# Optimization experiments

Measured on AMD Instinct MI355X. Metric: run time of the kernel, lower is better.

The kernel has to match this reference:

```python
import jax, jax.numpy as jnp
import numpy as np

IN_FEAT = 512
D_FEAT = 512
N_HEAD = 8
EPS = 1e-5
NEG = -1e9


def setup_inputs() -> dict:
    key = jax.random.key(0)
    ks = jax.random.split(key, 12)
    B, C, T = 8, IN_FEAT, 2048
    s_in = 1.0 / np.sqrt(IN_FEAT)
    s_d = 1.0 / np.sqrt(D_FEAT)
    return {
        "x": jax.random.normal(ks[0], (B, C, T), dtype=jnp.float32),
        "gamma": jnp.ones((IN_FEAT,), dtype=jnp.float32),
        "beta": jnp.zeros((IN_FEAT,), dtype=jnp.float32),
        "wq": jax.random.uniform(ks[1], (IN_FEAT, D_FEAT), jnp.float32, -s_in, s_in),
        "bq": jax.random.uniform(ks[2], (D_FEAT,), jnp.float32, -s_in, s_in),
        "wk": jax.random.uniform(ks[3], (IN_FEAT, D_FEAT), jnp.float32, -s_in, s_in),
        "bk": jax.random.uniform(ks[4], (D_FEAT,), jnp.float32, -s_in, s_in),
        "wv": jax.random.uniform(ks[5], (IN_FEAT, D_FEAT), jnp.float32, -s_in, s_in),
        "bv": jax.random.uniform(ks[6], (D_FEAT,), jnp.float32, -s_in, s_in),
        "wo": jax.random.uniform(ks[7], (D_FEAT, IN_FEAT), jnp.float32, -s_d, s_d),
        "bo": jax.random.uniform(ks[8], (IN_FEAT,), jnp.float32, -s_d, s_d),
    }


def reference(x, gamma, beta, wq, bq, wk, bk, wv, bv, wo, bo):
    # x: (B, Cin, T)
    resi = x
    h = jnp.swapaxes(x, -2, -1)  # (B, T, Cin)
    mu = jnp.mean(h, axis=-1, keepdims=True)
    var = jnp.mean(jnp.square(h - mu), axis=-1, keepdims=True)
    h = (h - mu) / jnp.sqrt(var + EPS) * gamma + beta

    B, T, _ = h.shape
    dh = D_FEAT // N_HEAD
    scale = np.sqrt(dh).astype(np.float32)

    def split_heads(y):  # (B,T,D) -> (B,H,T,dh)
        return jnp.swapaxes(y.reshape(B, T, N_HEAD, dh), 1, 2)

    q = split_heads(h @ wq + bq)
    k = split_heads(h @ wk + bk)
    v = split_heads(h @ wv + bv)

    scores = jnp.einsum('bhqd,bhkd->bhqk', q, k) / scale  # (B,H,T,T)
    mask = jnp.triu(jnp.ones((T, T), dtype=scores.dtype), k=1)  # strict upper
    scores = scores + NEG * mask
    attn = jax.nn.softmax(scores, axis=-1)
    ctx = jnp.einsum('bhqk,bhkd->bhqd', attn, v)  # (B,H,T,dh)
    ctx = jnp.swapaxes(ctx, 1, 2).reshape(B, T, D_FEAT)
    out = jnp.swapaxes(ctx @ wo + bo, -2, -1)  # (B, Cin, T)
    return resi + out
```

## Files before the change

kernel.cpp:

```cpp
#include <hip/hip_runtime.h>
#include <hip/hip_bf16.h>

#define BB 8
#define TT 2048
#define CC 512
#define DD 512
#define HH 8
#define DH 64

typedef __bf16 bf16x8 __attribute__((ext_vector_type(8)));
typedef __bf16 bf16x4 __attribute__((ext_vector_type(4)));
typedef float  f32x4  __attribute__((ext_vector_type(4)));

static __device__ __forceinline__ bf16x8 concat4(bf16x4 a, bf16x4 b) {
    bf16x8 r;
    #pragma unroll
    for (int i = 0; i < 4; ++i) { r[i] = a[i]; r[i + 4] = b[i]; }
    return r;
}

__global__ __launch_bounds__(256) void ln_kernel(
    const float* __restrict__ x, const float* __restrict__ gamma,
    const float* __restrict__ beta, __hip_bfloat16* __restrict__ h)
{
    const int b  = blockIdx.x >> 6;
    const int t0 = (blockIdx.x & 63) * 32;
    const int tid = threadIdx.x;
    const int tl = tid & 31;
    const int part = tid >> 5;

    const float* xb = x + (size_t)b * CC * TT;

    float sum = 0.f, sq = 0.f;
    for (int ci = 0; ci < 64; ++ci) {
        int c = part * 64 + ci;
        float v = xb[(size_t)c * TT + t0 + tl];
        sum += v; sq += v * v;
    }
    __shared__ float sA[8][32], sB[8][32];
    sA[part][tl] = sum; sB[part][tl] = sq;
    __syncthreads();
    __shared__ float s_mu[32], s_rstd[32];
    if (part == 0) {
        float s = 0.f, q = 0.f;
        for (int p = 0; p < 8; ++p) { s += sA[p][tl]; q += sB[p][tl]; }
        float mu  = s * (1.0f / 512.0f);
        float var = q * (1.0f / 512.0f) - mu * mu;
        s_mu[tl] = mu;
        s_rstd[tl] = rsqrtf(var + 1e-5f);
    }
    __syncthreads();

    const float mu = s_mu[tl], rstd = s_rstd[tl];
    __shared__ __hip_bfloat16 tileT[32][72];

    for (int chunk = 0; chunk < 8; ++chunk) {
        int cb = chunk * 64 + part * 8;
        #pragma unroll
        for (int j = 0; j < 8; ++j) {
            int c = cb + j;
            float v = xb[(size_t)c * TT + t0 + tl];
            float nv = (v - mu) * rstd * gamma[c] + beta[c];
            tileT[tl][part * 8 + j] = __float2bfloat16(nv);
        }
        __syncthreads();
        int cl = tid & 63, tw = tid >> 6;
        #pragma unroll
        for (int k = 0; k < 8; ++k) {
            int t = tw + k * 4;
            h[((size_t)(b * TT + t0 + t)) * CC + chunk * 64 + cl] = tileT[t][cl];
        }
        __syncthreads();
    }
}

__global__ __launch_bounds__(256) void prepack_w4(
    const float* __restrict__ w0, const float* __restrict__ w1,
    const float* __restrict__ w2, const float* __restrict__ w3,
    __hip_bfloat16* __restrict__ o0, __hip_bfloat16* __restrict__ o1,
    __hip_bfloat16* __restrict__ o2, __hip_bfloat16* __restrict__ o3)
{
    const float* w; __hip_bfloat16* wt;
    switch (blockIdx.y) {
        case 0: w = w0; wt = o0; break;
        case 1: w = w1; wt = o1; break;
        case 2: w = w2; wt = o2; break;
        default: w = w3; wt = o3; break;
    }
    __shared__ float tile[32][33];
    const int bx = blockIdx.x & 15;
    const int by = blockIdx.x >> 4;
    const int lx = threadIdx.x & 31, ly = threadIdx.x >> 5;
    #pragma unroll
    for (int i = 0; i < 4; ++i) {
        int k = by * 32 + ly + i * 8;
        tile[ly + i * 8][lx] = w[(size_t)k * 512 + bx * 32 + lx];
    }
    __syncthreads();
    #pragma unroll
    for (int i = 0; i < 4; ++i) {
        int n = bx * 32 + ly + i * 8;
        wt[(size_t)n * 512 + by * 32 + lx] = __float2bfloat16(tile[lx][ly + i * 8]);
    }
}

__global__ __launch_bounds__(256) void qkv_gemm(
    const __hip_bfloat16* __restrict__ A,
    const __hip_bfloat16* __restrict__ wtq, const __hip_bfloat16* __restrict__ wtk,
    const __hip_bfloat16* __restrict__ wtv,
    const float* __restrict__ bq, const float* __restrict__ bk,
    const float* __restrict__ bv,
    __hip_bfloat16* __restrict__ qo, __hip_bfloat16* __restrict__ ko,
    __hip_bfloat16* __restrict__ vt)
{
    const int m0 = blockIdx.x * 128;
    const int n0 = blockIdx.y * 128;
    const __hip_bfloat16* WT; const float* bias; __hip_bfloat16* out;
    if (blockIdx.z == 0)      { WT = wtq; bias = bq; out = qo; }
    else if (blockIdx.z == 1) { WT = wtk; bias = bk; out = ko; }
    else                      { WT = wtv; bias = bv; out = vt; }
    const float sc = (blockIdx.z == 0) ? 0.18033688011112042f : 1.0f;

    __shared__ __hip_bfloat16 As[2][128][40];
    __shared__ __hip_bfloat16 Bs[2][128][40];
    __shared__ float eps[4][16][17];

    const int tid = threadIdx.x;
    const int wave = tid >> 6, lane = tid & 63;
    const int quad = lane >> 4, l16 = lane & 15;
    const int wy = wave >> 1, wx = wave & 1;

    const int srow = tid >> 2;
    const int skof = (tid & 3) * 8;

    f32x4 acc[4][4] = {};
    bf16x8 areg[2], breg[2];

    #pragma unroll
    for (int i = 0; i < 2; ++i) {
        int r = srow + i * 64;
        areg[i] = *reinterpret_cast<const bf16x8*>(&A[(size_t)(m0 + r) * 512 + skof]);
        breg[i] = *reinterpret_cast<const bf16x8*>(&WT[(size_t)(n0 + r) * 512 + skof]);
    }
    #pragma unroll
    for (int i = 0; i < 2; ++i) {
        int r = srow + i * 64;
        *reinterpret_cast<bf16x8*>(&As[0][r][skof]) = areg[i];
        *reinterpret_cast<bf16x8*>(&Bs[0][r][skof]) = breg[i];
    }
    __syncthreads();

    for (int kt = 0; kt < 512; kt += 32) {
        const int cur = (kt >> 5) & 1;
        const bool havenext = (kt + 32 < 512);
        if (havenext) {
            #pragma unroll
            for (int i = 0; i < 2; ++i) {
                int r = srow + i * 64;
                areg[i] = *reinterpret_cast<const bf16x8*>(
                    &A[(size_t)(m0 + r) * 512 + kt + 32 + skof]);
                breg[i] = *reinterpret_cast<const bf16x8*>(
                    &WT[(size_t)(n0 + r) * 512 + kt + 32 + skof]);
            }
        }
        bf16x8 af[4], bfr[4];
        #pragma unroll
        for (int mt = 0; mt < 4; ++mt)
            af[mt] = *reinterpret_cast<const bf16x8*>(&As[cur][wy * 64 + mt * 16 + l16][quad * 8]);
        #pragma unroll
        for (int nt = 0; nt < 4; ++nt)
            bfr[nt] = *reinterpret_cast<const bf16x8*>(&Bs[cur][wx * 64 + nt * 16 + l16][quad * 8]);
        #pragma unroll
        for (int mt = 0; mt < 4; ++mt)
            #pragma unroll
            for (int nt = 0; nt < 4; ++nt)
                acc[mt][nt] = __builtin_amdgcn_mfma_f32_16x16x32_bf16(
                    af[mt], bfr[nt], acc[mt][nt], 0, 0, 0);
        if (havenext) {
            #pragma unroll
            for (int i = 0; i < 2; ++i) {
                int r = srow + i * 64;
                *reinterpret_cast<bf16x8*>(&As[cur ^ 1][r][skof]) = areg[i];
                *reinterpret_cast<bf16x8*>(&Bs[cur ^ 1][r][skof]) = breg[i];
            }
        }
        __syncthreads();
    }

    if (blockIdx.z != 2) {
        #pragma unroll
        for (int nt = 0; nt < 4; ++nt) {
            int n = n0 + wx * 64 + nt * 16 + l16;
            int hh = n >> 6, di = n & 63;
            float bval = bias[n];
            #pragma unroll
            for (int mt = 0; mt < 4; ++mt) {
                #pragma unroll
                for (int r = 0; r < 4; ++r) {
                    int m = m0 + wy * 64 + mt * 16 + quad * 4 + r;
                    int b = m >> 11, t = m & 2047;
                    out[((size_t)((b * HH + hh) * TT + t)) * DH + di] =
                        __float2bfloat16((acc[mt][nt][r] + bval) * sc);
                }
            }
        }
    } else {
        #pragma unroll
        for (int mt = 0; mt < 4; ++mt) {
            int mbase = m0 + wy * 64 + mt * 16;
            #pragma unroll
            for (int nt = 0; nt < 4; ++nt) {
                int ncol = n0 + wx * 64 + nt * 16 + l16;
                float bval = bias[ncol];
                #pragma unroll
                for (int r = 0; r < 4; ++r)
                    eps[wave][quad * 4 + r][l16] = acc[mt][nt][r] + bval;
                #pragma unroll
                for (int pass = 0; pass < 4; ++pass) {
                    int nl = pass * 4 + quad;
                    int n = n0 + wx * 64 + nt * 16 + nl;
                    int hh = n >> 6, di = n & 63;
                    int m = mbase + l16;
                    int b = m >> 11, t = m & 2047;
                    out[((size_t)((b * HH + hh) * DH + di)) * TT + t] =
                        __float2bfloat16(eps[wave][l16][nl]);
                }
            }
        }
    }
}

static __device__ __forceinline__ void attn_tile(
    const __hip_bfloat16 (*Ksb)[72], const __hip_bfloat16 (*Vtsb)[72],
    int k0, int q0, int wave, int quad, int l16,
    const bf16x8 (&qf)[2][2], f32x4 (&o_acc)[4][2], float (&l_run)[2])
{
    f32x4 s[2][4];
    #pragma unroll
    for (int nt = 0; nt < 4; ++nt) {
        bf16x8 kf0 = *reinterpret_cast<const bf16x8*>(&Ksb[nt * 16 + l16][quad * 8]);
        bf16x8 kf1 = *reinterpret_cast<const bf16x8*>(&Ksb[nt * 16 + l16][32 + quad * 8]);
        #pragma unroll
        for (int mt = 0; mt < 2; ++mt) {
            f32x4 z = {};
            z = __builtin_amdgcn_mfma_f32_16x16x32_bf16(kf0, qf[mt][0], z, 0, 0, 0);
            z = __builtin_amdgcn_mfma_f32_16x16x32_bf16(kf1, qf[mt][1], z, 0, 0, 0);
            s[mt][nt] = z;
        }
    }
    bf16x4 pt[2][4];
    #pragma unroll
    for (int mt = 0; mt < 2; ++mt) {
        const int qrow = q0 + wave * 32 + mt * 16 + l16;
        const bool fullun = (k0 + 63 <= q0 + wave * 32 + mt * 16);
        float lsum = 0.f;
        #pragma unroll
        for (int nt = 0; nt < 4; ++nt) {
            #pragma unroll
            for (int r = 0; r < 4; ++r) {
                float p = __builtin_amdgcn_exp2f(s[mt][nt][r]);
                if (!fullun) {
                    int key = k0 + nt * 16 + quad * 4 + r;
                    if (key > qrow) p = 0.f;
                }
                lsum += p;
                pt[mt][nt][r] = (__bf16)p;
            }
        }
        l_run[mt] += lsum;
    }
    #pragma unroll
    for (int cp = 0; cp < 2; ++cp) {
        bf16x8 pfr[2];
        #pragma unroll
        for (int mt = 0; mt < 2; ++mt)
            pfr[mt] = concat4(pt[mt][cp * 2], pt[mt][cp * 2 + 1]);
        #pragma unroll
        for (int dt = 0; dt < 4; ++dt) {
            bf16x4 va = *reinterpret_cast<const bf16x4*>(
                &Vtsb[dt * 16 + l16][cp * 32 + quad * 4]);
            bf16x4 vb = *reinterpret_cast<const bf16x4*>(
                &Vtsb[dt * 16 + l16][cp * 32 + 16 + quad * 4]);
            bf16x8 vf = concat4(va, vb);
            #pragma unroll
            for (int mt = 0; mt < 2; ++mt)
                o_acc[dt][mt] = __builtin_amdgcn_mfma_f32_16x16x32_bf16(
                    vf, pfr[mt], o_acc[dt][mt], 0, 0, 0);
        }
    }
}

__global__ __launch_bounds__(256, 2) void attn_kernel(
    const __hip_bfloat16* __restrict__ Q, const __hip_bfloat16* __restrict__ K,
    const __hip_bfloat16* __restrict__ Vt, __hip_bfloat16* __restrict__ ctx)
{
    const int xi = blockIdx.x;
    const int bh = blockIdx.y;
    const int q0h = (15 - xi) * 128;
    const int q0l = xi * 128;
    const __hip_bfloat16* Qb  = Q  + (size_t)bh * TT * DH;
    const __hip_bfloat16* Kb  = K  + (size_t)bh * TT * DH;
    const __hip_bfloat16* Vtb = Vt + (size_t)bh * DH * TT;

    const int tid = threadIdx.x, wave = tid >> 6, lane = tid & 63;
    const int quad = lane >> 4, l16 = lane & 15;

    __shared__ __hip_bfloat16 Ks[2][64][72];
    __shared__ __hip_bfloat16 Vts[2][64][72];

    bf16x8 qfh[2][2], qfl[2][2];
    #pragma unroll
    for (int mt = 0; mt < 2; ++mt) {
        int rh = q0h + wave * 32 + mt * 16 + l16;
        int rl = q0l + wave * 32 + mt * 16 + l16;
        #pragma unroll
        for (int st = 0; st < 2; ++st) {
            qfh[mt][st] = *reinterpret_cast<const bf16x8*>(
                &Qb[(size_t)rh * DH + st * 32 + quad * 8]);
            qfl[mt][st] = *reinterpret_cast<const bf16x8*>(
                &Qb[(size_t)rl * DH + st * 32 + quad * 8]);
        }
    }

    f32x4 oh[4][2] = {}, ol[4][2] = {};
    float lh[2] = {0.f, 0.f}, ll[2] = {0.f, 0.f};

    const int rr = tid >> 3;
    const int co = (tid & 7) * 8;

    bf16x8 kreg[2], vreg[2];
    #pragma unroll
    for (int i = 0; i < 2; ++i) {
        int r2 = rr + i * 32;
        kreg[i] = *reinterpret_cast<const bf16x8*>(&Kb[(size_t)r2 * DH + co]);
        vreg[i] = *reinterpret_cast<const bf16x8*>(&Vtb[(size_t)r2 * TT + co]);
    }
    #pragma unroll
    for (int i = 0; i < 2; ++i) {
        int r2 = rr + i * 32;
        *reinterpret_cast<bf16x8*>(&Ks[0][r2][co]) = kreg[i];
        *reinterpret_cast<bf16x8*>(&Vts[0][r2][co]) = vreg[i];
    }
    __syncthreads();

    const int nsteps = q0h / 64 + 2;
    for (int step = 0; step < nsteps; ++step) {
        const int k0 = step * 64;
        const int cur = step & 1;
        const bool havenext = (step + 1 < nsteps);
        if (havenext) {
            const int kn = k0 + 64;
            #pragma unroll
            for (int i = 0; i < 2; ++i) {
                int r2 = rr + i * 32;
                kreg[i] = *reinterpret_cast<const bf16x8*>(
                    &Kb[(size_t)(kn + r2) * DH + co]);
                vreg[i] = *reinterpret_cast<const bf16x8*>(
                    &Vtb[(size_t)r2 * TT + kn + co]);
            }
        }
        if (k0 <= q0h + wave * 32 + 31)
            attn_tile(Ks[cur], Vts[cur], k0, q0h, wave, quad, l16, qfh, oh, lh);
        if (k0 <= q0l + wave * 32 + 31)
            attn_tile(Ks[cur], Vts[cur], k0, q0l, wave, quad, l16, qfl, ol, ll);
        if (havenext) {
            const int nxt = cur ^ 1;
            #pragma unroll
            for (int i = 0; i < 2; ++i) {
                int r2 = rr + i * 32;
                *reinterpret_cast<bf16x8*>(&Ks[nxt][r2][co]) = kreg[i];
                *reinterpret_cast<bf16x8*>(&Vts[nxt][r2][co]) = vreg[i];
            }
        }
        __syncthreads();
    }

    float invh[2], invl[2];
    #pragma unroll
    for (int mt = 0; mt < 2; ++mt) {
        float a = lh[mt];
        a += __shfl_xor(a, 16, 64); a += __shfl_xor(a, 32, 64);
        invh[mt] = 1.0f / a;
        float c = ll[mt];
        c += __shfl_xor(c, 16, 64); c += __shfl_xor(c, 32, 64);
        invl[mt] = 1.0f / c;
    }

    const int b = bh >> 3, hh = bh & 7;
    #pragma unroll
    for (int mt = 0; mt < 2; ++mt) {
        int th = q0h + wave * 32 + mt * 16 + l16;
        int tl2 = q0l + wave * 32 + mt * 16 + l16;
        #pragma unroll
        for (int dt = 0; dt < 4; ++dt) {
            bf16x4 pa, pb;
            #pragma unroll
            for (int r = 0; r < 4; ++r) {
                pa[r] = (__bf16)(oh[dt][mt][r] * invh[mt]);
                pb[r] = (__bf16)(ol[dt][mt][r] * invl[mt]);
            }
            *reinterpret_cast<bf16x4*>(
                &ctx[((size_t)(b * TT + th)) * DD + hh * DH + dt * 16 + quad * 4]) = pa;
            *reinterpret_cast<bf16x4*>(
                &ctx[((size_t)(b * TT + tl2)) * DD + hh * DH + dt * 16 + quad * 4]) = pb;
        }
    }
}

__global__ __launch_bounds__(256) void oproj_gemm(
    const __hip_bfloat16* __restrict__ WT, const __hip_bfloat16* __restrict__ Actx,
    const float* __restrict__ bo, const float* __restrict__ xres,
    float* __restrict__ outp)
{
    const int m0 = blockIdx.x * 128;
    const int n0 = blockIdx.y * 128;

    __shared__ __hip_bfloat16 As[2][128][40];
    __shared__ __hip_bfloat16 Bs[2][128][40];

    const int tid = threadIdx.x;
    const int wave = tid >> 6, lane = tid & 63;
    const int quad = lane >> 4, l16 = lane & 15;
    const int wy = wave >> 1, wx = wave & 1;

    const int srow = tid >> 2;
    const int skof = (tid & 3) * 8;

    f32x4 acc[4][4] = {};
    bf16x8 areg[2], breg[2];

    #pragma unroll
    for (int i = 0; i < 2; ++i) {
        int r = srow + i * 64;
        areg[i] = *reinterpret_cast<const bf16x8*>(&WT[(size_t)(m0 + r) * 512 + skof]);
        breg[i] = *reinterpret_cast<const bf16x8*>(&Actx[(size_t)(n0 + r) * 512 + skof]);
    }
    #pragma unroll
    for (int i = 0; i < 2; ++i) {
        int r = srow + i * 64;
        *reinterpret_cast<bf16x8*>(&As[0][r][skof]) = areg[i];
        *reinterpret_cast<bf16x8*>(&Bs[0][r][skof]) = breg[i];
    }
    __syncthreads();

    for (int kt = 0; kt < 512; kt += 32) {
        const int cur = (kt >> 5) & 1;
        const bool havenext = (kt + 32 < 512);
        if (havenext) {
            #pragma unroll
            for (int i = 0; i < 2; ++i) {
                int r = srow + i * 64;
                areg[i] = *reinterpret_cast<const bf16x8*>(
                    &WT[(size_t)(m0 + r) * 512 + kt + 32 + skof]);
                breg[i] = *reinterpret_cast<const bf16x8*>(
                    &Actx[(size_t)(n0 + r) * 512 + kt + 32 + skof]);
            }
        }
        bf16x8 af[4], bfr[4];
        #pragma unroll
        for (int mt = 0; mt < 4; ++mt)
            af[mt] = *reinterpret_cast<const bf16x8*>(&As[cur][wy * 64 + mt * 16 + l16][quad * 8]);
        #pragma unroll
        for (int nt = 0; nt < 4; ++nt)
            bfr[nt] = *reinterpret_cast<const bf16x8*>(&Bs[cur][wx * 64 + nt * 16 + l16][quad * 8]);
        #pragma unroll
        for (int mt = 0; mt < 4; ++mt)
            #pragma unroll
            for (int nt = 0; nt < 4; ++nt)
                acc[mt][nt] = __builtin_amdgcn_mfma_f32_16x16x32_bf16(
                    af[mt], bfr[nt], acc[mt][nt], 0, 0, 0);
        if (havenext) {
            #pragma unroll
            for (int i = 0; i < 2; ++i) {
                int r = srow + i * 64;
                *reinterpret_cast<bf16x8*>(&As[cur ^ 1][r][skof]) = areg[i];
                *reinterpret_cast<bf16x8*>(&Bs[cur ^ 1][r][skof]) = breg[i];
            }
        }
        __syncthreads();
    }

    #pragma unroll
    for (int mt = 0; mt < 4; ++mt) {
        #pragma unroll
        for (int nt = 0; nt < 4; ++nt) {
            int tg = n0 + wx * 64 + nt * 16 + l16;
            int b = tg >> 11, t = tg & 2047;
            #pragma unroll
            for (int r = 0; r < 4; ++r) {
                int c = m0 + wy * 64 + mt * 16 + quad * 4 + r;
                size_t oi = ((size_t)(b * CC + c)) * TT + t;
                outp[oi] = xres[oi] + acc[mt][nt][r] + bo[c];
            }
        }
    }
}

extern "C" void kernel_launch(void* const* d_in, const int* in_sizes, int n_in,
                              void* d_out, int out_size, void* d_ws, size_t ws_size,
                              hipStream_t stream)
{
    const float* x     = (const float*)d_in[0];
    const float* gamma = (const float*)d_in[1];
    const float* beta  = (const float*)d_in[2];
    const float* wq    = (const float*)d_in[3];
    const float* bq    = (const float*)d_in[4];
    const float* wk    = (const float*)d_in[5];
    const float* bk    = (const float*)d_in[6];
    const float* wv    = (const float*)d_in[7];
    const float* bv    = (const float*)d_in[8];
    const float* wo    = (const float*)d_in[9];
    const float* bo    = (const float*)d_in[10];
    float* out = (float*)d_out;

    char* ws = (char*)d_ws;
    const size_t sz_big = (size_t)BB * TT * DD * sizeof(__hip_bfloat16);
    __hip_bfloat16* hbf = (__hip_bfloat16*)ws; ws += sz_big;
    __hip_bfloat16* qb  = (__hip_bfloat16*)ws; ws += sz_big;
    __hip_bfloat16* kb  = (__hip_bfloat16*)ws; ws += sz_big;
    __hip_bfloat16* vtb = (__hip_bfloat16*)ws; ws += sz_big;
    __hip_bfloat16* ctx = (__hip_bfloat16*)ws; ws += sz_big;
    const size_t sz_w = (size_t)512 * 512 * sizeof(__hip_bfloat16);
    __hip_bfloat16* wtq = (__hip_bfloat16*)ws; ws += sz_w;
    __hip_bfloat16* wtk = (__hip_bfloat16*)ws; ws += sz_w;
    __hip_bfloat16* wtv = (__hip_bfloat16*)ws; ws += sz_w;
    __hip_bfloat16* wto = (__hip_bfloat16*)ws; ws += sz_w;

    prepack_w4<<<dim3(256, 4), 256, 0, stream>>>(wq, wk, wv, wo,
                                                 wtq, wtk, wtv, wto);

    ln_kernel<<<BB * (TT / 32), 256, 0, stream>>>(x, gamma, beta, hbf);

    qkv_gemm<<<dim3(BB * TT / 128, DD / 128, 3), 256, 0, stream>>>(
        hbf, wtq, wtk, wtv, bq, bk, bv, qb, kb, vtb);

    attn_kernel<<<dim3(8, BB * HH), 256, 0, stream>>>(qb, kb, vtb, ctx);

    oproj_gemm<<<dim3(CC / 128, BB * TT / 128), 256, 0, stream>>>(
        wto, ctx, bo, x, out);
}
```

Before: 241.7 us.

## Use direct global-to-LDS loads in GEMMs, cache LN input, pair attention tiles

The QKV and output-projection GEMMs now load tiles straight into LDS with global_load_lds on a single unpadded buffer, replacing the register-staged double buffer. This drops VGPR staging but leaves global loads unoverlapped with MFMA work and may add LDS bank conflicts. The layernorm kernel keeps x in shared memory so the second global read is avoided, at the cost of 64KB of LDS per block. Attention interleaves the high and low query tiles in one routine so each K/V fragment load is shared and more MFMAs are independent.

```diff
diff --git a/kernel.cpp b/kernel.cpp
--- a/kernel.cpp
+++ b/kernel.cpp
@@ -19,6 +19,12 @@
     return r;
 }
 
+static __device__ __forceinline__ void async_ld16(const void* g, void* l) {
+    __builtin_amdgcn_global_load_lds(
+        (const __attribute__((address_space(1))) void*)g,
+        (__attribute__((address_space(3))) void*)l, 16, 0, 0);
+}
+
 __global__ __launch_bounds__(256) void ln_kernel(
     const float* __restrict__ x, const float* __restrict__ gamma,
     const float* __restrict__ beta, __hip_bfloat16* __restrict__ h)
@@ -31,10 +37,13 @@
 
     const float* xb = x + (size_t)b * CC * TT;
 
+    __shared__ float xs[512][32];
     float sum = 0.f, sq = 0.f;
+    #pragma unroll 8
     for (int ci = 0; ci < 64; ++ci) {
         int c = part * 64 + ci;
         float v = xb[(size_t)c * TT + t0 + tl];
+        xs[c][tl] = v;
         sum += v; sq += v * v;
     }
     __shared__ float sA[8][32], sB[8][32];
@@ -59,8 +68,7 @@
         #pragma unroll
         for (int j = 0; j < 8; ++j) {
             int c = cb + j;
-            float v = xb[(size_t)c * TT + t0 + tl];
-            float nv = (v - mu) * rstd * gamma[c] + beta[c];
+            float nv = (xs[c][tl] - mu) * rstd * gamma[c] + beta[c];
             tileT[tl][part * 8 + j] = __float2bfloat16(nv);
         }
         __syncthreads();
@@ -121,8 +129,8 @@
     else                      { WT = wtv; bias = bv; out = vt; }
     const float sc = (blockIdx.z == 0) ? 0.18033688011112042f : 1.0f;
 
-    __shared__ __hip_bfloat16 As[2][128][40];
-    __shared__ __hip_bfloat16 Bs[2][128][40];
+    __shared__ __hip_bfloat16 As[128][32];
+    __shared__ __hip_bfloat16 Bs[128][32];
     __shared__ float eps[4][16][17];
 
     const int tid = threadIdx.x;
@@ -130,60 +138,33 @@
     const int quad = lane >> 4, l16 = lane & 15;
     const int wy = wave >> 1, wx = wave & 1;
 
-    const int srow = tid >> 2;
-    const int skof = (tid & 3) * 8;
+    const int lrow = lane >> 2;
+    const int lcol = (lane & 3) * 8;
 
     f32x4 acc[4][4] = {};
-    bf16x8 areg[2], breg[2];
-
-    #pragma unroll
-    for (int i = 0; i < 2; ++i) {
-        int r = srow + i * 64;
-        areg[i] = *reinterpret_cast<const bf16x8*>(&A[(size_t)(m0 + r) * 512 + skof]);
-        breg[i] = *reinterpret_cast<const bf16x8*>(&WT[(size_t)(n0 + r) * 512 + skof]);
-    }
-    #pragma unroll
-    for (int i = 0; i < 2; ++i) {
-        int r = srow + i * 64;
-        *reinterpret_cast<bf16x8*>(&As[0][r][skof]) = areg[i];
-        *reinterpret_cast<bf16x8*>(&Bs[0][r][skof]) = breg[i];
-    }
-    __syncthreads();
 
     for (int kt = 0; kt < 512; kt += 32) {
-        const int cur = (kt >> 5) & 1;
-        const bool havenext = (kt + 32 < 512);
-        if (havenext) {
-            #pragma unroll
-            for (int i = 0; i < 2; ++i) {
-                int r = srow + i * 64;
-                areg[i] = *reinterpret_cast<const bf16x8*>(
-                    &A[(size_t)(m0 + r) * 512 + kt + 32 + skof]);
-                breg[i] = *reinterpret_cast<const bf16x8*>(
-                    &WT[(size_t)(n0 + r) * 512 + kt + 32 + skof]);
-            }
-        }
+        #pragma unroll
+        for (int i = 0; i < 2; ++i) {
+            int rbase = wave * 32 + i * 16;
+            int row = rbase + lrow;
+            async_ld16(&A[(size_t)(m0 + row) * 512 + kt + lcol], &As[rbase][0]);
+            async_ld16(&WT[(size_t)(n0 + row) * 512 + kt + lcol], &Bs[rbase][0]);
+        }
+        __syncthreads();
         bf16x8 af[4], bfr[4];
         #pragma unroll
         for (int mt = 0; mt < 4; ++mt)
-            af[mt] = *reinterpret_cast<const bf16x8*>(&As[cur][wy * 64 + mt * 16 + l16][quad * 8]);
+            af[mt] = *reinterpret_cast<const bf16x8*>(&As[wy * 64 + mt * 16 + l16][quad * 8]);
         #pragma unroll
         for (int nt = 0; nt < 4; ++nt)
-            bfr[nt] = *reinterpret_cast<const bf16x8*>(&Bs[cur][wx * 64 + nt * 16 + l16][quad * 8]);
+            bfr[nt] = *reinterpret_cast<const bf16x8*>(&Bs[wx * 64 + nt * 16 + l16][quad * 8]);
         #pragma unroll
         for (int mt = 0; mt < 4; ++mt)
             #pragma unroll
             for (int nt = 0; nt < 4; ++nt)
                 acc[mt][nt] = __builtin_amdgcn_mfma_f32_16x16x32_bf16(
                     af[mt], bfr[nt], acc[mt][nt], 0, 0, 0);
-        if (havenext) {
-            #pragma unroll
-            for (int i = 0; i < 2; ++i) {
-                int r = srow + i * 64;
-                *reinterpret_cast<bf16x8*>(&As[cur ^ 1][r][skof]) = areg[i];
-                *reinterpret_cast<bf16x8*>(&Bs[cur ^ 1][r][skof]) = breg[i];
-            }
-        }
         __syncthreads();
     }
 
@@ -230,51 +211,89 @@
     }
 }
 
-static __device__ __forceinline__ void attn_tile(
+static __device__ __forceinline__ void exp_phase(
+    const f32x4 (&s)[2][4], bf16x4 (&pt)[2][4], float (&lr)[2],
+    int k0, int q0, int wave, int quad, int l16)
+{
+    #pragma unroll
+    for (int mt = 0; mt < 2; ++mt) {
+        float lsum = 0.f;
+        if (k0 + 63 <= q0 + wave * 32 + mt * 16) {
+            #pragma unroll
+            for (int nt = 0; nt < 4; ++nt) {
+                #pragma unroll
+                for (int r = 0; r < 4; ++r) {
+                    float p = __builtin_amdgcn_exp2f(s[mt][nt][r]);
+                    lsum += p;
+                    pt[mt][nt][r] = (__bf16)p;
+                }
+            }
+        } else {
+            const int qrow = q0 + wave * 32 + mt * 16 + l16;
+            #pragma unroll
+            for (int nt = 0; nt < 4; ++nt) {
+                #pragma unroll
+                for (int r = 0; r < 4; ++r) {
+                    float p = __builtin_amdgcn_exp2f(s[mt][nt][r]);
+                    int key = k0 + nt * 16 + quad * 4 + r;
+                    if (key > qrow) p = 0.f;
+                    lsum += p;
+                    pt[mt][nt][r] = (__bf16)p;
+                }
+            }
+        }
+        lr[mt] += lsum;
+    }
+}
+
+static __device__ __forceinline__ void attn_tile_pair(
     const __hip_bfloat16 (*Ksb)[72], const __hip_bfloat16 (*Vtsb)[72],
-    int k0, int q0, int wave, int quad, int l16,
-    const bf16x8 (&qf)[2][2], f32x4 (&o_acc)[4][2], float (&l_run)[2])
-{
-    f32x4 s[2][4];
+    int k0, int q0h, int q0l, int wave, int quad, int l16,
+    const bf16x8 (&qfh)[2][2], const bf16x8 (&qfl)[2][2],
+    f32x4 (&oh)[4][2], f32x4 (&ol)[4][2],
+    float (&lh)[2], float (&ll)[2], bool doh, bool dol)
+{
+    f32x4 sh[2][4], sl[2][4];
     #pragma unroll
     for (int nt = 0; nt < 4; ++nt) {
         bf16x8 kf0 = *reinterpret_cast<const bf16x8*>(&Ksb[nt * 16 + l16][quad * 8]);
         bf16x8 kf1 = *reinterpret_cast<const bf16x8*>(&Ksb[nt * 16 + l16][32 + quad * 8]);
-        #pragma unroll
-        for (int mt = 0; mt < 2; ++mt) {
-            f32x4 z = {};
-            z = __builtin_amdgcn_mfma_f32_16x16x32_bf16(kf0, qf[mt][0], z, 0, 0, 0);
-            z = __builtin_amdgcn_mfma_f32_16x16x32_bf16(kf1, qf[mt][1], z, 0, 0, 0);
-            s[mt][nt] = z;
-        }
-    }
-    bf16x4 pt[2][4];
-    #pragma unroll
-    for (int mt = 0; mt < 2; ++mt) {
-        const int qrow = q0 + wave * 32 + mt * 16 + l16;
-        const bool fullun = (k0 + 63 <= q0 + wave * 32 + mt * 16);
-        float lsum = 0.f;
-        #pragma unroll
-        for (int nt = 0; nt < 4; ++nt) {
-            #pragma unroll
-            for (int r = 0; r < 4; ++r) {
-                float p = __builtin_amdgcn_exp2f(s[mt][nt][r]);
-                if (!fullun) {
-                    int key = k0 + nt * 16 + quad * 4 + r;
-                    if (key > qrow) p = 0.f;
-                }
-                lsum += p;
-                pt[mt][nt][r] = (__bf16)p;
-            }
-        }
-        l_run[mt] += lsum;
-    }
+        if (doh) {
+            #pragma unroll
+            for (int mt = 0; mt < 2; ++mt) {
+                f32x4 z = {};
+                z = __builtin_amdgcn_mfma_f32_16x16x32_bf16(kf0, qfh[mt][0], z, 0, 0, 0);
+                z = __builtin_amdgcn_mfma_f32_16x16x32_bf16(kf1, qfh[mt][1], z, 0, 0, 0);
+                sh[mt][nt] = z;
+            }
+        }
+        if (dol) {
+            #pragma unroll
+            for (int mt = 0; mt < 2; ++mt) {
+                f32x4 z = {};
+                z = __builtin_amdgcn_mfma_f32_16x16x32_bf16(kf0, qfl[mt][0], z, 0, 0, 0);
+                z = __builtin_amdgcn_mfma_f32_16x16x32_bf16(kf1, qfl[mt][1], z, 0, 0, 0);
+                sl[mt][nt] = z;
+            }
+        }
+    }
+    bf16x4 pth[2][4], ptl[2][4];
+    if (doh) exp_phase(sh, pth, lh, k0, q0h, wave, quad, l16);
+    if (dol) exp_phase(sl, ptl, ll, k0, q0l, wave, quad, l16);
+
     #pragma unroll
     for (int cp = 0; cp < 2; ++cp) {
-        bf16x8 pfr[2];
-        #pragma unroll
-        for (int mt = 0; mt < 2; ++mt)
-            pfr[mt] = concat4(pt[mt][cp * 2], pt[mt][cp * 2 + 1]);
+        bf16x8 pfh[2], pfl[2];
+        if (doh) {
+            #pragma unroll
+            for (int mt = 0; mt < 2; ++mt)
+                pfh[mt] = concat4(pth[mt][cp * 2], pth[mt][cp * 2 + 1]);
+        }
+        if (dol) {
+            #pragma unroll
+            for (int mt = 0; mt < 2; ++mt)
+                pfl[mt] = concat4(ptl[mt][cp * 2], ptl[mt][cp * 2 + 1]);
+        }
         #pragma unroll
         for (int dt = 0; dt < 4; ++dt) {
             bf16x4 va = *reinterpret_cast<const bf16x4*>(
@@ -282,10 +301,18 @@
             bf16x4 vb = *reinterpret_cast<const bf16x4*>(
                 &Vtsb[dt * 16 + l16][cp * 32 + 16 + quad * 4]);
             bf16x8 vf = concat4(va, vb);
-            #pragma unroll
-            for (int mt = 0; mt < 2; ++mt)
-                o_acc[dt][mt] = __builtin_amdgcn_mfma_f32_16x16x32_bf16(
-                    vf, pfr[mt], o_acc[dt][mt], 0, 0, 0);
+            if (doh) {
+                #pragma unroll
+                for (int mt = 0; mt < 2; ++mt)
+                    oh[dt][mt] = __builtin_amdgcn_mfma_f32_16x16x32_bf16(
+                        vf, pfh[mt], oh[dt][mt], 0, 0, 0);
+            }
+            if (dol) {
+                #pragma unroll
+                for (int mt = 0; mt < 2; ++mt)
+                    ol[dt][mt] = __builtin_amdgcn_mfma_f32_16x16x32_bf16(
+                        vf, pfl[mt], ol[dt][mt], 0, 0, 0);
+            }
         }
     }
 }
@@ -359,10 +386,11 @@
                     &Vtb[(size_t)r2 * TT + kn + co]);
             }
         }
-        if (k0 <= q0h + wave * 32 + 31)
-            attn_tile(Ks[cur], Vts[cur], k0, q0h, wave, quad, l16, qfh, oh, lh);
-        if (k0 <= q0l + wave * 32 + 31)
-            attn_tile(Ks[cur], Vts[cur], k0, q0l, wave, quad, l16, qfl, ol, ll);
+        const bool doh = (k0 <= q0h + wave * 32 + 31);
+        const bool dol = (k0 <= q0l + wave * 32 + 31);
+        if (doh || dol)
+            attn_tile_pair(Ks[cur], Vts[cur], k0, q0h, q0l, wave, quad, l16,
+                           qfh, qfl, oh, ol, lh, ll, doh, dol);
         if (havenext) {
             const int nxt = cur ^ 1;
             #pragma unroll
@@ -415,68 +443,41 @@
     const int m0 = blockIdx.x * 128;
     const int n0 = blockIdx.y * 128;
 
-    __shared__ __hip_bfloat16 As[2][128][40];
-    __shared__ __hip_bfloat16 Bs[2][128][40];
+    __shared__ __hip_bfloat16 As[128][32];
+    __shared__ __hip_bfloat16 Bs[128][32];
 
     const int tid = threadIdx.x;
     const int wave = tid >> 6, lane = tid & 63;
     const int quad = lane >> 4, l16 = lane & 15;
     const int wy = wave >> 1, wx = wave & 1;
 
-    const int srow = tid >> 2;
-    const int skof = (tid & 3) * 8;
+    const int lrow = lane >> 2;
+    const int lcol = (lane & 3) * 8;
 
     f32x4 acc[4][4] = {};
-    bf16x8 areg[2], breg[2];
-
-    #pragma unroll
-    for (int i = 0; i < 2; ++i) {
-        int r = srow + i * 64;
-        areg[i] = *reinterpret_cast<const bf16x8*>(&WT[(size_t)(m0 + r) * 512 + skof]);
-        breg[i] = *reinterpret_cast<const bf16x8*>(&Actx[(size_t)(n0 + r) * 512 + skof]);
-    }
-    #pragma unroll
-    for (int i = 0; i < 2; ++i) {
-        int r = srow + i * 64;
-        *reinterpret_cast<bf16x8*>(&As[0][r][skof]) = areg[i];
-        *reinterpret_cast<bf16x8*>(&Bs[0][r][skof]) = breg[i];
-    }
-    __syncthreads();
 
     for (int kt = 0; kt < 512; kt += 32) {
-        const int cur = (kt >> 5) & 1;
-        const bool havenext = (kt + 32 < 512);
-        if (havenext) {
-            #pragma unroll
-            for (int i = 0; i < 2; ++i) {
-                int r = srow + i * 64;
-                areg[i] = *reinterpret_cast<const bf16x8*>(
-                    &WT[(size_t)(m0 + r) * 512 + kt + 32 + skof]);
-                breg[i] = *reinterpret_cast<const bf16x8*>(
-                    &Actx[(size_t)(n0 + r) * 512 + kt + 32 + skof]);
-            }
-        }
+        #pragma unroll
+        for (int i = 0; i < 2; ++i) {
+            int rbase = wave * 32 + i * 16;
+            int row = rbase + lrow;
+            async_ld16(&WT[(size_t)(m0 + row) * 512 + kt + lcol], &As[rbase][0]);
+            async_ld16(&Actx[(size_t)(n0 + row) * 512 + kt + lcol], &Bs[rbase][0]);
+        }
+        __syncthreads();
         bf16x8 af[4], bfr[4];
         #pragma unroll
         for (int mt = 0; mt < 4; ++mt)
-            af[mt] = *reinterpret_cast<const bf16x8*>(&As[cur][wy * 64 + mt * 16 + l16][quad * 8]);
+            af[mt] = *reinterpret_cast<const bf16x8*>(&As[wy * 64 + mt * 16 + l16][quad * 8]);
         #pragma unroll
         for (int nt = 0; nt < 4; ++nt)
-            bfr[nt] = *reinterpret_cast<const bf16x8*>(&Bs[cur][wx * 64 + nt * 16 + l16][quad * 8]);
+            bfr[nt] = *reinterpret_cast<const bf16x8*>(&Bs[wx * 64 + nt * 16 + l16][quad * 8]);
         #pragma unroll
         for (int mt = 0; mt < 4; ++mt)
             #pragma unroll
             for (int nt = 0; nt < 4; ++nt)
                 acc[mt][nt] = __builtin_amdgcn_mfma_f32_16x16x32_bf16(
                     af[mt], bfr[nt], acc[mt][nt], 0, 0, 0);
-        if (havenext) {
-            #pragma unroll
-            for (int i = 0; i < 2; ++i) {
-                int r = srow + i * 64;
-                *reinterpret_cast<bf16x8*>(&As[cur ^ 1][r][skof]) = areg[i];
-                *reinterpret_cast<bf16x8*>(&Bs[cur ^ 1][r][skof]) = breg[i];
-            }
-        }
         __syncthreads();
     }
 
```

Result: no change. 240.6 us (-0.5%).
